# Kernel tuning notes

Hardware: AMD Instinct MI355X
Metric: run time of the kernel (lower is better)

## Reference

```python
import jax, jax.numpy as jnp
import numpy as np
from jax import lax

N_CHANNELS = 16
FIRE_RATE = 0.5
STEP_SIZE = 1.0
ALPHA_THRESH = 0.1

_identity = np.array([[0.0, 0.0, 0.0], [0.0, 1.0, 0.0], [0.0, 0.0, 0.0]], np.float32)
_dx = np.array([[-0.125, 0.0, 0.125], [-0.25, 0.0, 0.25], [-0.125, 0.0, 0.125]], np.float32)
_dy = _dx.T
# angle = 0.0 -> cos=1, sin=0 -> filters unchanged
_all_filters = np.stack((_identity, _dx, _dy))              # (3,3,3)
_filters = np.tile(_all_filters, (N_CHANNELS, 1, 1))[:, None]  # (48,1,3,3) OIHW
PERCEIVE_FILTERS = jnp.asarray(_filters)


def wrap_edges(x):
    # circular pad of 1 on H and W; x: [B,C,H,W]
    return jnp.pad(x, ((0, 0), (0, 0), (1, 1), (1, 1)), mode='wrap')


def living_mask(x):
    alpha = x[:, 3:4]                                   # [B,1,H,W]
    pooled = lax.reduce_window(wrap_edges(alpha), -jnp.inf, lax.max,
                               (1, 1, 3, 3), (1, 1, 1, 1), 'VALID')
    return pooled > ALPHA_THRESH                        # [B,1,H,W] bool


def perceive(x):
    # depthwise 3x3 with 3 filters per channel, circular boundary
    return lax.conv_general_dilated(
        wrap_edges(x), PERCEIVE_FILTERS,
        window_strides=(1, 1), padding='VALID',
        dimension_numbers=('NCHW', 'OIHW', 'NCHW'),
        feature_group_count=N_CHANNELS)                 # [B,48,H,W]


def setup_inputs() -> dict:
    key = jax.random.key(0)
    k1, k2, k3, k4 = jax.random.split(key, 4)
    B, C, H, W = 16, N_CHANNELS, 256, 256
    x = jax.random.uniform(k1, (B, C, H, W), dtype=jnp.float32)
    rand_vals = jax.random.uniform(k2, (B, 1, H, W), dtype=jnp.float32)
    w1 = jax.random.normal(k3, (3 * C, 128), dtype=jnp.float32) * 0.05
    b1 = jnp.zeros((128,), jnp.float32)
    w2 = jax.random.normal(k4, (128, 16), dtype=jnp.float32) * 0.05
    b2 = jnp.zeros((16,), jnp.float32)
    return {"x": x, "rand_vals": rand_vals, "w1": w1, "b1": b1, "w2": w2, "b2": b2}


def reference(x, rand_vals, w1, b1, w2, b2):
    pre_life = living_mask(x)
    p = perceive(x)                                      # [B,48,H,W]
    h = jax.nn.relu(jnp.einsum('bchw,cd->bdhw', p, w1) + b1[None, :, None, None])
    dx = (jnp.einsum('bchw,cd->bdhw', h, w2) + b2[None, :, None, None]) * STEP_SIZE
    update_mask = (rand_vals < FIRE_RATE).astype(x.dtype)  # [B,1,H,W]
    x = x + dx * update_mask
    post_life = living_mask(x)
    life = (pre_life & post_life).astype(x.dtype)
    return x * life
```

## Files before the change

kernel.cpp:

```cpp
#include <hip/hip_runtime.h>
#include <hip/hip_bf16.h>

typedef __attribute__((ext_vector_type(8))) short bf16x8;
typedef __attribute__((ext_vector_type(4))) short bf16x4;
typedef __attribute__((ext_vector_type(4))) float f32x4;
typedef __attribute__((ext_vector_type(4))) unsigned int u32x4;
typedef __attribute__((ext_vector_type(2))) unsigned int u32x2;

#define NC   16
#define IMG  (256*256)

#define P_OFF   0
#define W1_OFF  28672
#define W2_OFF  43008
#define B1_OFF  47360
#define B2_OFF  47872
#define LDS_TOT 47936
#define BNC_SZ  9472
#define BNC_DX  4352

static __device__ __forceinline__ unsigned short f2bf(float f) {
    union { __hip_bfloat16 h; unsigned short u; } cv;
    cv.h = __float2bfloat16(f);
    return cv.u;
}
static __device__ __forceinline__ unsigned int packbf2(float a, float b) {
    return (unsigned int)f2bf(a) | ((unsigned int)f2bf(b) << 16);
}
static __device__ __forceinline__ f32x4 mfma_bf16_16x16x16(bf16x4 a, bf16x4 b, f32x4 c) {
#if __has_builtin(__builtin_amdgcn_mfma_f32_16x16x16bf16_1k)
    return __builtin_amdgcn_mfma_f32_16x16x16bf16_1k(a, b, c, 0, 0, 0);
#else
    f32x4 d;
    asm("v_mfma_f32_16x16x16_bf16 %0, %1, %2, %3" : "=v"(d) : "v"(a), "v"(b), "v"(c));
    return d;
#endif
}

__global__ __launch_bounds__(256, 3) void nca_update_mfma(
    const float* __restrict__ x, const float* __restrict__ rand_vals,
    const float* __restrict__ w1, const float* __restrict__ b1,
    const float* __restrict__ w2, const float* __restrict__ b2,
    float* __restrict__ out, float* __restrict__ alpha_ws)
{
    __shared__ __align__(16) unsigned char lds[LDS_TOT];
    const int t = threadIdx.x;

    const int wg = (blockIdx.x & 7) * 512 + (blockIdx.x >> 3);
    const int b  = wg >> 8;
    const int h  = wg & 255;
    const int w  = t;

    #pragma unroll
    for (int i = 0; i < 24; i++) {
        int idx = i*256 + t;
        int n = idx & 127, k = idx >> 7;
        *(unsigned short*)(lds + W1_OFF + n*112 + k*2) = f2bf(w1[k*128 + n]);
    }
    #pragma unroll
    for (int i = 0; i < 8; i++) {
        int idx = i*256 + t;
        int c = idx & 15, k = idx >> 4;
        *(unsigned short*)(lds + W2_OFF + c*272 + k*2) = f2bf(w2[k*16 + c]);
    }
    if (t < 128) *(float*)(lds + B1_OFF + t*4) = b1[t];
    if (t < 16)  *(float*)(lds + B2_OFF + t*4) = b2[t];

    const int hm = (h + 255) & 255, hp = (h + 1) & 255;
    const int wm = (w + 255) & 255, wp = (w + 1) & 255;
    const float* xb = x + (size_t)b * NC * IMG;
    float p[48], premax = 0.0f;
    #pragma unroll
    for (int c = 0; c < 16; c++) {
        const float* xcp = xb + c * IMG;
        const float* r0 = xcp + hm*256;
        const float* r1 = xcp + h *256;
        const float* r2 = xcp + hp*256;
        float a00=r0[wm],a01=r0[w],a02=r0[wp];
        float a10=r1[wm],a11=r1[w],a12=r1[wp];
        float a20=r2[wm],a21=r2[w],a22=r2[wp];
        p[3*c+0]=a11;
        p[3*c+1]=0.125f*(a02-a00)+0.25f*(a12-a10)+0.125f*(a22-a20);
        p[3*c+2]=0.125f*(a20-a00)+0.25f*(a21-a01)+0.125f*(a22-a02);
        if (c == 3)
            premax = fmaxf(fmaxf(fmaxf(a00,a01),fmaxf(a02,a10)),
                     fmaxf(fmaxf(a11,a12),fmaxf(fmaxf(a20,a21),a22)));
    }
    {
        unsigned int pk[24];
        #pragma unroll
        for (int j = 0; j < 24; j++) pk[j] = packbf2(p[2*j], p[2*j+1]);
        u32x4* pv = (u32x4*)(lds + P_OFF + t*112);
        #pragma unroll
        for (int j = 0; j < 6; j++) {
            u32x4 v = {pk[4*j], pk[4*j+1], pk[4*j+2], pk[4*j+3]};
            pv[j] = v;
        }
    }
    __syncthreads();

    const int wv = t >> 6, l15 = t & 15, lg = (t >> 4) & 3;

    bf16x8 A1a[8]; bf16x4 A1b[8];
    #pragma unroll
    for (int mt = 0; mt < 8; mt++) {
        const unsigned char* r = lds + W1_OFF + (mt*16 + l15)*112;
        A1a[mt] = *(const bf16x8*)(r + lg*16);
        A1b[mt] = *(const bf16x4*)(r + 64 + lg*8);
    }
    bf16x8 Bpa[4]; bf16x4 Bpb[4];
    #pragma unroll
    for (int pt = 0; pt < 4; pt++) {
        const unsigned char* r = lds + P_OFF + (wv*64 + pt*16 + l15)*112;
        Bpa[pt] = *(const bf16x8*)(r + lg*16);
        Bpb[pt] = *(const bf16x4*)(r + 64 + lg*8);
    }
    bf16x8 A2[4];
    #pragma unroll
    for (int kt = 0; kt < 4; kt++)
        A2[kt] = *(const bf16x8*)(lds + W2_OFF + l15*272 + kt*64 + lg*16);
    f32x4 b2frag = *(const f32x4*)(lds + B2_OFF + lg*16);

    asm volatile("s_waitcnt lgkmcnt(0)" ::: "memory");
    __builtin_amdgcn_sched_barrier(0);
    __syncthreads();

    unsigned char* hb  = lds + wv*BNC_SZ;
    unsigned char* dxb = lds + wv*BNC_SZ + BNC_DX;

    #pragma unroll
    for (int pt = 0; pt < 4; pt++) {
        f32x4 hacc[8];
        #pragma unroll
        for (int mt = 0; mt < 8; mt++) {
            f32x4 a = *(const f32x4*)(lds + B1_OFF + (mt*16 + lg*4)*4);
            a = __builtin_amdgcn_mfma_f32_16x16x32_bf16(A1a[mt], Bpa[pt], a, 0,0,0);
            a = mfma_bf16_16x16x16(A1b[mt], Bpb[pt], a);
            hacc[mt] = a;
        }
        asm volatile("s_waitcnt lgkmcnt(0)" ::: "memory");
        __builtin_amdgcn_sched_barrier(0);
        #pragma unroll
        for (int mt = 0; mt < 8; mt++) {
            float h0 = fmaxf(hacc[mt][0], 0.f), h1 = fmaxf(hacc[mt][1], 0.f);
            float h2 = fmaxf(hacc[mt][2], 0.f), h3 = fmaxf(hacc[mt][3], 0.f);
            u32x2 pk2 = {packbf2(h0, h1), packbf2(h2, h3)};
            *(u32x2*)(hb + l15*272 + mt*32 + lg*8) = pk2;
        }
        asm volatile("s_waitcnt lgkmcnt(0)" ::: "memory");
        __builtin_amdgcn_sched_barrier(0);
        f32x4 acc2 = b2frag;
        #pragma unroll
        for (int kt = 0; kt < 4; kt++) {
            bf16x8 Bh = *(const bf16x8*)(hb + l15*272 + kt*64 + lg*16);
            acc2 = __builtin_amdgcn_mfma_f32_16x16x32_bf16(A2[kt], Bh, acc2, 0,0,0);
        }
        *(f32x4*)(dxb + (pt*16 + l15)*80 + lg*16) = acc2;
    }
    asm volatile("s_waitcnt lgkmcnt(0)" ::: "memory");
    __builtin_amdgcn_sched_barrier(0);

    const unsigned char* myd = dxb + (t & 63)*80;
    float dxv[16];
    *(f32x4*)&dxv[0]  = *(const f32x4*)(myd +  0);
    *(f32x4*)&dxv[4]  = *(const f32x4*)(myd + 16);
    *(f32x4*)&dxv[8]  = *(const f32x4*)(myd + 32);
    *(f32x4*)&dxv[12] = *(const f32x4*)(myd + 48);

    const float rv = rand_vals[b*IMG + h*256 + w];
    const float fm = (rv < 0.5f) ? 1.0f : 0.0f;
    const float lifep = (premax > 0.1f) ? 1.0f : 0.0f;

    const float* xctr = xb + h*256 + w;
    const float xa = xctr[3*IMG];
    alpha_ws[b*IMG + h*256 + w] = fmaf(dxv[3], fm, xa);

    float* ob = out + (size_t)b*NC*IMG + h*256 + w;
    #pragma unroll
    for (int c = 0; c < 16; c++)
        ob[c*IMG] = fmaf(dxv[c], fm, xctr[c*IMG]) * lifep;
}

__global__ __launch_bounds__(256) void nca_postmask(
    const float* __restrict__ alpha_ws, float* __restrict__ out)
{
    const int wg = (blockIdx.x & 7) * 512 + (blockIdx.x >> 3);
    const int b  = wg >> 8;
    const int h  = wg & 255;
    const int w  = threadIdx.x;
    const int hm = (h + 255) & 255, hp = (h + 1) & 255;
    const int wm = (w + 255) & 255, wp = (w + 1) & 255;

    const float* na = alpha_ws + b*IMG;
    const float* n0 = na + hm*256;
    const float* n1 = na + h *256;
    const float* n2 = na + hp*256;
    float post = fmaxf(fmaxf(fmaxf(n0[wm],n0[w]),fmaxf(n0[wp],n1[wm])),
                 fmaxf(fmaxf(n1[w],n1[wp]),fmaxf(fmaxf(n2[wm],n2[w]),n2[wp])));
    if (!(post > 0.1f)) {
        float* ob = out + (size_t)b*NC*IMG + h*256 + w;
        #pragma unroll
        for (int c = 0; c < 16; c++) ob[c*IMG] = 0.0f;
    }
}

extern "C" void kernel_launch(void* const* d_in, const int* in_sizes, int n_in,
                              void* d_out, int out_size, void* d_ws, size_t ws_size,
                              hipStream_t stream) {
    const float* x         = (const float*)d_in[0];
    const float* rand_vals = (const float*)d_in[1];
    const float* w1        = (const float*)d_in[2];
    const float* b1        = (const float*)d_in[3];
    const float* w2        = (const float*)d_in[4];
    const float* b2        = (const float*)d_in[5];
    float* out      = (float*)d_out;
    float* alpha_ws = (float*)d_ws;

    const int grid = 16 * 256;
    nca_update_mfma<<<grid, 256, 0, stream>>>(x, rand_vals, w1, b1, w2, b2,
                                              out, alpha_ws);
    nca_postmask<<<grid, 256, 0, stream>>>(alpha_ws, out);
}
```

Measured before the change: 62.75 us.

## Shrink LDS footprint and registers to raise occupancy to four blocks per CU

Cuts the shared-memory budget from about 47.9KB to 40KB. W2 and both biases now come from global memory or registers instead of LDS, the W1 row stride is tightened, and the per-wave dx staging is stored as bf16 instead of f32. W1 fragments are reloaded from LDS inside the MFMA loop rather than held in registers. The 16-channel stencil loads are double-buffered two channels at a time so fewer registers are live. Together these target four resident blocks per CU instead of three, at the cost of extra LDS reads per tile and some precision lost on dx.

Result: slower. 96.01 us (+53.0%).

```diff
diff --git a/kernel.cpp b/kernel.cpp
--- a/kernel.cpp
+++ b/kernel.cpp
@@ -10,14 +10,12 @@
 #define NC   16
 #define IMG  (256*256)
 
-#define P_OFF   0
-#define W1_OFF  28672
-#define W2_OFF  43008
-#define B1_OFF  47360
-#define B2_OFF  47872
-#define LDS_TOT 47936
-#define BNC_SZ  9472
-#define BNC_DX  4352
+#define P_STRIDE  112
+#define W1_OFF    28672
+#define W1_STRIDE 96
+#define LDS_TOT   40960
+#define CHUNK     7168
+#define DX_OFF    4352
 
 static __device__ __forceinline__ unsigned short f2bf(float f) {
     union { __hip_bfloat16 h; unsigned short u; } cv;
@@ -26,6 +24,12 @@
 }
 static __device__ __forceinline__ unsigned int packbf2(float a, float b) {
     return (unsigned int)f2bf(a) | ((unsigned int)f2bf(b) << 16);
+}
+static __device__ __forceinline__ float bflo(unsigned int u) {
+    union { unsigned int i; float f; } c; c.i = u << 16; return c.f;
+}
+static __device__ __forceinline__ float bfhi(unsigned int u) {
+    union { unsigned int i; float f; } c; c.i = u & 0xffff0000u; return c.f;
 }
 static __device__ __forceinline__ f32x4 mfma_bf16_16x16x16(bf16x4 a, bf16x4 b, f32x4 c) {
 #if __has_builtin(__builtin_amdgcn_mfma_f32_16x16x16bf16_1k)
@@ -37,14 +41,15 @@
 #endif
 }
 
-__global__ __launch_bounds__(256, 3) void nca_update_mfma(
+__global__ __launch_bounds__(256, 4) void nca_update_mfma(
     const float* __restrict__ x, const float* __restrict__ rand_vals,
     const float* __restrict__ w1, const float* __restrict__ b1,
     const float* __restrict__ w2, const float* __restrict__ b2,
     float* __restrict__ out, float* __restrict__ alpha_ws)
 {
     __shared__ __align__(16) unsigned char lds[LDS_TOT];
-    const int t = threadIdx.x;
+    const int t   = threadIdx.x;
+    const int l15 = t & 15, lg = (t >> 4) & 3, wv = t >> 6;
 
     const int wg = (blockIdx.x & 7) * 512 + (blockIdx.x >> 3);
     const int b  = wg >> 8;
@@ -53,132 +58,157 @@
 
     #pragma unroll
     for (int i = 0; i < 24; i++) {
-        int idx = i*256 + t;
-        int n = idx & 127, k = idx >> 7;
-        *(unsigned short*)(lds + W1_OFF + n*112 + k*2) = f2bf(w1[k*128 + n]);
-    }
-    #pragma unroll
-    for (int i = 0; i < 8; i++) {
-        int idx = i*256 + t;
-        int c = idx & 15, k = idx >> 4;
-        *(unsigned short*)(lds + W2_OFF + c*272 + k*2) = f2bf(w2[k*16 + c]);
-    }
-    if (t < 128) *(float*)(lds + B1_OFF + t*4) = b1[t];
-    if (t < 16)  *(float*)(lds + B2_OFF + t*4) = b2[t];
+        int k = (t & 15) + 16 * (i % 3);
+        int n = (t >> 4) + 16 * (i / 3);
+        *(unsigned short*)(lds + W1_OFF + n*W1_STRIDE + k*2) = f2bf(w1[k*128 + n]);
+    }
 
     const int hm = (h + 255) & 255, hp = (h + 1) & 255;
     const int wm = (w + 255) & 255, wp = (w + 1) & 255;
     const float* xb = x + (size_t)b * NC * IMG;
-    float p[48], premax = 0.0f;
-    #pragma unroll
-    for (int c = 0; c < 16; c++) {
-        const float* xcp = xb + c * IMG;
-        const float* r0 = xcp + hm*256;
-        const float* r1 = xcp + h *256;
-        const float* r2 = xcp + hp*256;
-        float a00=r0[wm],a01=r0[w],a02=r0[wp];
-        float a10=r1[wm],a11=r1[w],a12=r1[wp];
-        float a20=r2[wm],a21=r2[w],a22=r2[wp];
-        p[3*c+0]=a11;
-        p[3*c+1]=0.125f*(a02-a00)+0.25f*(a12-a10)+0.125f*(a22-a20);
-        p[3*c+2]=0.125f*(a20-a00)+0.25f*(a21-a01)+0.125f*(a22-a02);
-        if (c == 3)
-            premax = fmaxf(fmaxf(fmaxf(a00,a01),fmaxf(a02,a10)),
-                     fmaxf(fmaxf(a11,a12),fmaxf(fmaxf(a20,a21),a22)));
-    }
+    const int r0o = hm*256, r1o = h*256, r2o = hp*256;
+
+    const float rv = rand_vals[b*IMG + r1o + w];
+
+    float buf[2][18];
+    unsigned int pk[24];
+    float premax = 0.0f;
+
+    #pragma unroll
+    for (int cc = 0; cc < 2; cc++) {
+        const float* xc_ = xb + cc*IMG;
+        float* bu = &buf[0][cc*9];
+        bu[0]=xc_[r0o+wm]; bu[1]=xc_[r0o+w]; bu[2]=xc_[r0o+wp];
+        bu[3]=xc_[r1o+wm]; bu[4]=xc_[r1o+w]; bu[5]=xc_[r1o+wp];
+        bu[6]=xc_[r2o+wm]; bu[7]=xc_[r2o+w]; bu[8]=xc_[r2o+wp];
+    }
+    #pragma unroll
+    for (int pr = 0; pr < 8; pr++) {
+        if (pr < 7) {
+            #pragma unroll
+            for (int cc = 0; cc < 2; cc++) {
+                const float* xc_ = xb + ((pr+1)*2 + cc)*IMG;
+                float* bu = &buf[(pr+1)&1][cc*9];
+                bu[0]=xc_[r0o+wm]; bu[1]=xc_[r0o+w]; bu[2]=xc_[r0o+wp];
+                bu[3]=xc_[r1o+wm]; bu[4]=xc_[r1o+w]; bu[5]=xc_[r1o+wp];
+                bu[6]=xc_[r2o+wm]; bu[7]=xc_[r2o+w]; bu[8]=xc_[r2o+wp];
+            }
+        }
+        float pv[6];
+        #pragma unroll
+        for (int cc = 0; cc < 2; cc++) {
+            const float* a = &buf[pr&1][cc*9];
+            pv[cc*3+0] = a[4];
+            pv[cc*3+1] = 0.125f*(a[2]-a[0]) + 0.25f*(a[5]-a[3]) + 0.125f*(a[8]-a[6]);
+            pv[cc*3+2] = 0.125f*(a[6]-a[0]) + 0.25f*(a[7]-a[1]) + 0.125f*(a[8]-a[2]);
+            if (pr*2 + cc == 3)
+                premax = fmaxf(fmaxf(fmaxf(a[0],a[1]),fmaxf(a[2],a[3])),
+                         fmaxf(fmaxf(a[4],a[5]),fmaxf(fmaxf(a[6],a[7]),a[8])));
+        }
+        pk[pr*3+0] = packbf2(pv[0], pv[1]);
+        pk[pr*3+1] = packbf2(pv[2], pv[3]);
+        pk[pr*3+2] = packbf2(pv[4], pv[5]);
+    }
+
     {
-        unsigned int pk[24];
-        #pragma unroll
-        for (int j = 0; j < 24; j++) pk[j] = packbf2(p[2*j], p[2*j+1]);
-        u32x4* pv = (u32x4*)(lds + P_OFF + t*112);
+        u32x4* pvv = (u32x4*)(lds + t*P_STRIDE);
         #pragma unroll
         for (int j = 0; j < 6; j++) {
             u32x4 v = {pk[4*j], pk[4*j+1], pk[4*j+2], pk[4*j+3]};
-            pv[j] = v;
-        }
-    }
+            pvv[j] = v;
+        }
+    }
+
+    float a2raw[32];
+    #pragma unroll
+    for (int kt = 0; kt < 4; kt++)
+        #pragma unroll
+        for (int j = 0; j < 8; j++)
+            a2raw[kt*8+j] = w2[(kt*32 + lg*8 + j)*16 + l15];
+
     __syncthreads();
 
-    const int wv = t >> 6, l15 = t & 15, lg = (t >> 4) & 3;
-
-    bf16x8 A1a[8]; bf16x4 A1b[8];
-    #pragma unroll
-    for (int mt = 0; mt < 8; mt++) {
-        const unsigned char* r = lds + W1_OFF + (mt*16 + l15)*112;
-        A1a[mt] = *(const bf16x8*)(r + lg*16);
-        A1b[mt] = *(const bf16x4*)(r + 64 + lg*8);
-    }
+    bf16x8 A2[4];
+    #pragma unroll
+    for (int kt = 0; kt < 4; kt++) {
+        bf16x8 v;
+        #pragma unroll
+        for (int j = 0; j < 8; j++) v[j] = (short)f2bf(a2raw[kt*8+j]);
+        A2[kt] = v;
+    }
+    const f32x4 b2f = *(const f32x4*)(b2 + lg*4);
+
     bf16x8 Bpa[4]; bf16x4 Bpb[4];
     #pragma unroll
     for (int pt = 0; pt < 4; pt++) {
-        const unsigned char* r = lds + P_OFF + (wv*64 + pt*16 + l15)*112;
+        const unsigned char* r = lds + (wv*64 + pt*16 + l15)*P_STRIDE;
         Bpa[pt] = *(const bf16x8*)(r + lg*16);
         Bpb[pt] = *(const bf16x4*)(r + 64 + lg*8);
     }
-    bf16x8 A2[4];
-    #pragma unroll
-    for (int kt = 0; kt < 4; kt++)
-        A2[kt] = *(const bf16x8*)(lds + W2_OFF + l15*272 + kt*64 + lg*16);
-    f32x4 b2frag = *(const f32x4*)(lds + B2_OFF + lg*16);
 
     asm volatile("s_waitcnt lgkmcnt(0)" ::: "memory");
     __builtin_amdgcn_sched_barrier(0);
     __syncthreads();
 
-    unsigned char* hb  = lds + wv*BNC_SZ;
-    unsigned char* dxb = lds + wv*BNC_SZ + BNC_DX;
+    unsigned char* chunk = lds + wv*CHUNK;
 
     #pragma unroll
     for (int pt = 0; pt < 4; pt++) {
         f32x4 hacc[8];
         #pragma unroll
         for (int mt = 0; mt < 8; mt++) {
-            f32x4 a = *(const f32x4*)(lds + B1_OFF + (mt*16 + lg*4)*4);
-            a = __builtin_amdgcn_mfma_f32_16x16x32_bf16(A1a[mt], Bpa[pt], a, 0,0,0);
-            a = mfma_bf16_16x16x16(A1b[mt], Bpb[pt], a);
-            hacc[mt] = a;
+            const unsigned char* wr = lds + W1_OFF + (mt*16 + l15)*W1_STRIDE;
+            bf16x8 A1a = *(const bf16x8*)(wr + lg*16);
+            bf16x4 A1b = *(const bf16x4*)(wr + 64 + lg*8);
+            f32x4 acc = *(const f32x4*)(b1 + mt*16 + lg*4);
+            acc = __builtin_amdgcn_mfma_f32_16x16x32_bf16(A1a, Bpa[pt], acc, 0,0,0);
+            acc = mfma_bf16_16x16x16(A1b, Bpb[pt], acc);
+            hacc[mt] = acc;
         }
         asm volatile("s_waitcnt lgkmcnt(0)" ::: "memory");
         __builtin_amdgcn_sched_barrier(0);
         #pragma unroll
         for (int mt = 0; mt < 8; mt++) {
-            float h0 = fmaxf(hacc[mt][0], 0.f), h1 = fmaxf(hacc[mt][1], 0.f);
-            float h2 = fmaxf(hacc[mt][2], 0.f), h3 = fmaxf(hacc[mt][3], 0.f);
-            u32x2 pk2 = {packbf2(h0, h1), packbf2(h2, h3)};
-            *(u32x2*)(hb + l15*272 + mt*32 + lg*8) = pk2;
+            u32x2 hq = {packbf2(fmaxf(hacc[mt][0],0.f), fmaxf(hacc[mt][1],0.f)),
+                        packbf2(fmaxf(hacc[mt][2],0.f), fmaxf(hacc[mt][3],0.f))};
+            *(u32x2*)(chunk + l15*272 + mt*32 + lg*8) = hq;
         }
         asm volatile("s_waitcnt lgkmcnt(0)" ::: "memory");
         __builtin_amdgcn_sched_barrier(0);
-        f32x4 acc2 = b2frag;
+        f32x4 acc2 = b2f;
         #pragma unroll
         for (int kt = 0; kt < 4; kt++) {
-            bf16x8 Bh = *(const bf16x8*)(hb + l15*272 + kt*64 + lg*16);
+            bf16x8 Bh = *(const bf16x8*)(chunk + l15*272 + kt*64 + lg*16);
             acc2 = __builtin_amdgcn_mfma_f32_16x16x32_bf16(A2[kt], Bh, acc2, 0,0,0);
         }
-        *(f32x4*)(dxb + (pt*16 + l15)*80 + lg*16) = acc2;
+        u32x2 dq = {packbf2(acc2[0], acc2[1]), packbf2(acc2[2], acc2[3])};
+        *(u32x2*)(chunk + DX_OFF + (pt*16 + l15)*40 + lg*8) = dq;
     }
     asm volatile("s_waitcnt lgkmcnt(0)" ::: "memory");
     __builtin_amdgcn_sched_barrier(0);
 
-    const unsigned char* myd = dxb + (t & 63)*80;
+    const unsigned char* myd = chunk + DX_OFF + (t & 63)*40;
+    u32x2 q0 = *(const u32x2*)(myd +  0);
+    u32x2 q1 = *(const u32x2*)(myd +  8);
+    u32x2 q2 = *(const u32x2*)(myd + 16);
+    u32x2 q3 = *(const u32x2*)(myd + 24);
     float dxv[16];
-    *(f32x4*)&dxv[0]  = *(const f32x4*)(myd +  0);
-    *(f32x4*)&dxv[4]  = *(const f32x4*)(myd + 16);
-    *(f32x4*)&dxv[8]  = *(const f32x4*)(myd + 32);
-    *(f32x4*)&dxv[12] = *(const f32x4*)(myd + 48);
-
-    const float rv = rand_vals[b*IMG + h*256 + w];
-    const float fm = (rv < 0.5f) ? 1.0f : 0.0f;
+    dxv[0]=bflo(q0.x); dxv[1]=bfhi(q0.x); dxv[2]=bflo(q0.y); dxv[3]=bfhi(q0.y);
+    dxv[4]=bflo(q1.x); dxv[5]=bfhi(q1.x); dxv[6]=bflo(q1.y); dxv[7]=bfhi(q1.y);
+    dxv[8]=bflo(q2.x); dxv[9]=bfhi(q2.x); dxv[10]=bflo(q2.y); dxv[11]=bfhi(q2.y);
+    dxv[12]=bflo(q3.x); dxv[13]=bfhi(q3.x); dxv[14]=bflo(q3.y); dxv[15]=bfhi(q3.y);
+
+    const float fm    = (rv < 0.5f)     ? 1.0f : 0.0f;
     const float lifep = (premax > 0.1f) ? 1.0f : 0.0f;
 
-    const float* xctr = xb + h*256 + w;
+    const float* xctr = xb + r1o + w;
     const float xa = xctr[3*IMG];
-    alpha_ws[b*IMG + h*256 + w] = fmaf(dxv[3], fm, xa);
-
-    float* ob = out + (size_t)b*NC*IMG + h*256 + w;
+    alpha_ws[b*IMG + r1o + w] = fmaf(dxv[3], fm, xa);
+
+    float* ob = out + (size_t)b*NC*IMG + r1o + w;
     #pragma unroll
     for (int c = 0; c < 16; c++)
-        ob[c*IMG] = fmaf(dxv[c], fm, xctr[c*IMG]) * lifep;
+        ob[(size_t)c*IMG] = fmaf(dxv[c], fm, xctr[(size_t)c*IMG]) * lifep;
 }
 
 __global__ __launch_bounds__(256) void nca_postmask(
```
